# Optimization experiments

Measured on AMD Instinct MI355X. Metric: run time of the kernel, lower is better.

The kernel has to match this reference:

```python
import jax, jax.numpy as jnp
import numpy as np

B, T, C, H = 2, 2048, 1024, 16
HD = C // H  # head dim = 64


def setup_inputs() -> dict:
    key = jax.random.key(0)
    ks = jax.random.split(key, 5)
    s = 0.02  # GPT-style init scale for weights
    return {
        "x": jax.random.normal(ks[0], (B, T, C), dtype=jnp.float32),
        "Wq": jax.random.normal(ks[1], (C, C), dtype=jnp.float32) * s,
        "bq": jnp.zeros((C,), dtype=jnp.float32),
        "Wk": jax.random.normal(ks[2], (C, C), dtype=jnp.float32) * s,
        "bk": jnp.zeros((C,), dtype=jnp.float32),
        "Wv": jax.random.normal(ks[3], (C, C), dtype=jnp.float32) * s,
        "bv": jnp.zeros((C,), dtype=jnp.float32),
        "Wp": jax.random.normal(ks[4], (C, C), dtype=jnp.float32) * s,
        "bp": jnp.zeros((C,), dtype=jnp.float32),
    }


def reference(x, Wq, bq, Wk, bk, Wv, bv, Wp, bp):
    b, t, c = x.shape
    # torch nn.Linear: y = x @ W.T + b  (W is [out, in])
    def heads(W, bias):
        y = jnp.einsum("btc,oc->bto", x, W) + bias
        return y.reshape(b, t, H, HD).transpose(0, 2, 1, 3)  # [B,H,T,hd]

    q = heads(Wq, bq)
    k = heads(Wk, bk)
    v = heads(Wv, bv)

    scale = 1.0 / np.sqrt(HD).astype(np.float32)
    att = jnp.einsum("bhqd,bhkd->bhqk", q, k) * scale  # [B,H,T,T]
    causal = jnp.tril(jnp.ones((t, t), dtype=bool))
    att = jnp.where(causal[None, None], att, -jnp.inf)
    att = jax.nn.softmax(att, axis=-1)
    # attn_pdrop = 0.0 -> dropout is identity
    y = jnp.einsum("bhqk,bhkd->bhqd", att, v)  # [B,H,T,hd]
    y = y.transpose(0, 2, 1, 3).reshape(b, t, c)
    y = jnp.einsum("btc,oc->bto", y, Wp) + bp  # resid_pdrop = 0.0
    return y
```

## Files before the change

### kernel.cpp

```cpp
#include <hip/hip_runtime.h>
#include <hip/hip_bf16.h>

using bf16 = __hip_bfloat16;
typedef __attribute__((ext_vector_type(8))) short short8;
typedef __attribute__((ext_vector_type(4))) float floatx4;

#define B_  2
#define T_  2048
#define C_  1024
#define H_  16
#define HD_ 64
#define BT_ (B_*T_)
#define NX_ ((size_t)BT_*C_)
#define NW_ ((size_t)C_*C_)
#define PSTR 136
#define KSCQ 0.1803368801f

__device__ __forceinline__ void gl2lds16(const bf16* g, bf16* l) {
    __builtin_amdgcn_global_load_lds((const __attribute__((address_space(1))) unsigned int*)g,
                                     (__attribute__((address_space(3))) unsigned int*)l,
                                     16, 0, 0);
}

__global__ __launch_bounds__(256) void cvt_f32_bf16(
    const float* __restrict__ x,
    const float* __restrict__ Wq, const float* __restrict__ Wk,
    const float* __restrict__ Wv, const float* __restrict__ Wp,
    bf16* __restrict__ xb, bf16* __restrict__ wqb, bf16* __restrict__ wkb,
    bf16* __restrict__ wvb, bf16* __restrict__ wpb)
{
    size_t i4 = ((size_t)blockIdx.x * 256 + threadIdx.x) * 4;
    const float* src; bf16* dst; size_t off;
    if (i4 < NX_) { src = x; dst = xb; off = i4; }
    else {
        size_t j = i4 - NX_;
        int r = (int)(j >> 20);
        off = j & (NW_ - 1);
        src = (r==0) ? Wq : (r==1) ? Wk : (r==2) ? Wv : Wp;
        dst = (r==0) ? wqb : (r==1) ? wkb : (r==2) ? wvb : wpb;
    }
    float4 v = *(const float4*)(src + off);
    union { bf16 h[4]; uint2 u; } o;
    o.h[0] = __float2bfloat16(v.x); o.h[1] = __float2bfloat16(v.y);
    o.h[2] = __float2bfloat16(v.z); o.h[3] = __float2bfloat16(v.w);
    *(uint2*)(dst + off) = o.u;
}

__global__ __launch_bounds__(256) void qkv_gemm(
    const bf16* __restrict__ x,
    const bf16* __restrict__ Wq, const float* __restrict__ bq,
    const bf16* __restrict__ Wk, const float* __restrict__ bk,
    const bf16* __restrict__ Wv, const float* __restrict__ bv,
    bf16* __restrict__ qo, bf16* __restrict__ ko, bf16* __restrict__ vt)
{
    __shared__ __align__(16) bf16 As[128*32];
    __shared__ __align__(16) bf16 Bs[128*32];

    const int tid  = threadIdx.x;
    const int w    = tid >> 6, lane = tid & 63;
    const int g    = lane >> 4, c16 = lane & 15;
    const int wr   = w >> 1,    wc  = w & 1;
    const int mtile = blockIdx.x, ntile = blockIdx.y;
    const int wsel  = ntile >> 3;
    const bf16*  W    = (wsel==0) ? Wq : (wsel==1 ? Wk : Wv);
    const float* bias = (wsel==0) ? bq : (wsel==1 ? bk : bv);
    const float oscale = (wsel==0) ? KSCQ : 1.0f;
    const int nbase  = (ntile & 7) * 128;

    const bf16* ag = x + (size_t)(mtile*128)*C_;
    const bf16* bg = W + (size_t)nbase*C_;

    floatx4 acc[4][4] = {};

    for (int k0 = 0; k0 < C_; k0 += 32) {
        #pragma unroll
        for (int p = 0; p < 2; ++p) {
            int cb = p*256 + w*64;
            int c  = cb + lane;
            gl2lds16(ag + (size_t)(c>>2)*C_ + k0 + (c&3)*8, As + cb*8);
            gl2lds16(bg + (size_t)(c>>2)*C_ + k0 + (c&3)*8, Bs + cb*8);
        }
        __syncthreads();

        short8 af[4], bfr[4];
        #pragma unroll
        for (int i = 0; i < 4; ++i)
            af[i] = *(const short8*)(As + (wr*64 + i*16 + c16)*32 + g*8);
        #pragma unroll
        for (int j = 0; j < 4; ++j)
            bfr[j] = *(const short8*)(Bs + (wc*64 + j*16 + c16)*32 + g*8);
        #pragma unroll
        for (int i = 0; i < 4; ++i)
            #pragma unroll
            for (int j = 0; j < 4; ++j)
                acc[i][j] = __builtin_amdgcn_mfma_f32_16x16x32_bf16(af[i], bfr[j], acc[i][j], 0, 0, 0);
        __syncthreads();
    }

    #pragma unroll
    for (int i = 0; i < 4; ++i) {
        int m0 = mtile*128 + wr*64 + i*16 + g*4;
        #pragma unroll
        for (int j = 0; j < 4; ++j) {
            int n = nbase + wc*64 + j*16 + c16;
            float bvf = bias[n];
            if (wsel == 2) {
                int bb = m0 >> 11, t0 = m0 & (T_-1);
                int hh = n >> 6,  hd = n & 63;
                union { bf16 hv[4]; uint2 u; } tmp;
                #pragma unroll
                for (int r = 0; r < 4; ++r) tmp.hv[r] = __float2bfloat16(acc[i][j][r] + bvf);
                *(uint2*)(vt + ((size_t)((bb*H_ + hh)*64 + hd))*T_ + t0) = tmp.u;
            } else {
                bf16* dst = (wsel==0) ? qo : ko;
                #pragma unroll
                for (int r = 0; r < 4; ++r)
                    dst[(size_t)(m0+r)*C_ + n] = __float2bfloat16((acc[i][j][r] + bvf) * oscale);
            }
        }
    }
}

__global__ __launch_bounds__(256) void attn(
    const bf16* __restrict__ q, const bf16* __restrict__ k,
    const bf16* __restrict__ vt, bf16* __restrict__ y)
{
    __shared__ __align__(16) bf16 Ks[16*512];
    __shared__ __align__(16) bf16 Vs[16*512];
    __shared__ __align__(16) bf16 Ps[4][16*PSTR];

    const int tid = threadIdx.x, w = tid >> 6, lane = tid & 63;
    const int g = lane >> 4, c16 = lane & 15;
    const int jj = blockIdx.x, h = blockIdx.y, b = blockIdx.z;

    const bf16* kbase = k  + ((size_t)(b*T_))*C_ + h*64;
    const bf16* vbase = vt + ((size_t)(b*H_ + h))*64*T_;

    #pragma unroll 1
    for (int seg = 0; seg < 2; ++seg) {
        const int qt = seg ? jj : 31 - jj;
        const int qbase = qt*64 + w*16;
        const int nit = (qt + 2) >> 1;
        const int qglob = qbase + c16;

        short8 aq[2];
        #pragma unroll
        for (int kg = 0; kg < 2; ++kg)
            aq[kg] = *(const short8*)(q + ((size_t)(b*T_ + qglob))*C_ + h*64 + kg*32 + g*8);

        floatx4 accO[4] = {};
        float m_l = -1e30f, l_l = 0.f;

        for (int kt = 0; kt < nit; ++kt) {
            #pragma unroll
            for (int p = 0; p < 4; ++p) {
                int f = w*4 + p;
                int ctk = f >> 1, kg = f & 1;
                gl2lds16(kbase + (size_t)(kt*128 + ctk*16 + c16)*C_ + kg*32 + g*8, Ks + f*512);
                gl2lds16(vbase + (size_t)(p*16 + c16)*T_ + kt*128 + w*32 + g*8,    Vs + f*512);
            }
            __syncthreads();

            floatx4 s[8];
            #pragma unroll
            for (int ct = 0; ct < 8; ++ct) {
                floatx4 a = {0.f, 0.f, 0.f, 0.f};
                #pragma unroll
                for (int kg = 0; kg < 2; ++kg) {
                    short8 kb = *(const short8*)(Ks + (ct*2 + kg)*512 + lane*8);
                    a = __builtin_amdgcn_mfma_f32_16x16x32_bf16(kb, aq[kg], a, 0, 0, 0);
                }
                s[ct] = a;
            }

            if (kt == nit-1) {
                #pragma unroll
                for (int ct = 0; ct < 8; ++ct)
                    #pragma unroll
                    for (int r = 0; r < 4; ++r) {
                        int key = kt*128 + ct*16 + g*4 + r;
                        if (key > qglob) s[ct][r] = -1e30f;
                    }
            }

            float cm[8];
            #pragma unroll
            for (int ct = 0; ct < 8; ++ct)
                cm[ct] = fmaxf(fmaxf(s[ct][0], s[ct][1]), fmaxf(s[ct][2], s[ct][3]));
            float tmax = fmaxf(fmaxf(fmaxf(cm[0], cm[1]), fmaxf(cm[2], cm[3])),
                               fmaxf(fmaxf(cm[4], cm[5]), fmaxf(cm[6], cm[7])));
            tmax = fmaxf(tmax, __shfl_xor(tmax, 16));
            tmax = fmaxf(tmax, __shfl_xor(tmax, 32));
            float mn = fmaxf(m_l, tmax);
            float alpha = exp2f(m_l - mn);
            m_l = mn;

            float s0 = 0.f, s1 = 0.f, s2 = 0.f, s3 = 0.f;
            #pragma unroll
            for (int ct = 0; ct < 8; ++ct) {
                float p0 = exp2f(s[ct][0] - mn);
                float p1 = exp2f(s[ct][1] - mn);
                float p2 = exp2f(s[ct][2] - mn);
                float p3 = exp2f(s[ct][3] - mn);
                s0 += p0; s1 += p1; s2 += p2; s3 += p3;
                union { __hip_bfloat162 h2[2]; uint2 u; } pk;
                pk.h2[0] = __float22bfloat162_rn(float2{p0, p1});
                pk.h2[1] = __float22bfloat162_rn(float2{p2, p3});
                *(uint2*)(Ps[w] + c16*PSTR + ct*16 + g*4) = pk.u;
            }
            float tsum = (s0 + s1) + (s2 + s3);
            tsum += __shfl_xor(tsum, 16);
            tsum += __shfl_xor(tsum, 32);
            l_l = l_l*alpha + tsum;

            float ar[4];
            #pragma unroll
            for (int r = 0; r < 4; ++r) ar[r] = __shfl(alpha, g*4 + r);
            #pragma unroll
            for (int nt = 0; nt < 4; ++nt)
                #pragma unroll
                for (int r = 0; r < 4; ++r) accO[nt][r] *= ar[r];

            #pragma unroll
            for (int ks = 0; ks < 4; ++ks) {
                short8 pa = *(const short8*)(Ps[w] + c16*PSTR + ks*32 + g*8);
                #pragma unroll
                for (int nt = 0; nt < 4; ++nt) {
                    short8 vb = *(const short8*)(Vs + (ks*4 + nt)*512 + lane*8);
                    accO[nt] = __builtin_amdgcn_mfma_f32_16x16x32_bf16(pa, vb, accO[nt], 0, 0, 0);
                }
            }
            __syncthreads();
        }

        float ir[4];
        #pragma unroll
        for (int r = 0; r < 4; ++r) ir[r] = __builtin_amdgcn_rcpf(__shfl(l_l, g*4 + r));
        #pragma unroll
        for (int nt = 0; nt < 4; ++nt)
            #pragma unroll
            for (int r = 0; r < 4; ++r) {
                int row = qbase + g*4 + r;
                float o = accO[nt][r] * ir[r];
                y[((size_t)(b*T_ + row))*C_ + h*64 + nt*16 + c16] = __float2bfloat16(o);
            }
    }
}

__global__ __launch_bounds__(256) void proj_gemm(
    const bf16* __restrict__ yin, const bf16* __restrict__ Wp, const float* __restrict__ bp,
    float* __restrict__ out)
{
    __shared__ __align__(16) bf16 As[128*32];
    __shared__ __align__(16) bf16 Bs[128*32];

    const int tid = threadIdx.x;
    const int w = tid >> 6, lane = tid & 63;
    const int g = lane >> 4, c16 = lane & 15;
    const int wr = w >> 1, wc = w & 1;
    const int mtile = blockIdx.x, ntile = blockIdx.y;
    const int nbase = ntile * 128;

    const bf16* ag = yin + (size_t)(mtile*128)*C_;
    const bf16* bg = Wp  + (size_t)nbase*C_;

    floatx4 acc[4][4] = {};

    for (int k0 = 0; k0 < C_; k0 += 32) {
        #pragma unroll
        for (int p = 0; p < 2; ++p) {
            int cb = p*256 + w*64;
            int c  = cb + lane;
            gl2lds16(ag + (size_t)(c>>2)*C_ + k0 + (c&3)*8, As + cb*8);
            gl2lds16(bg + (size_t)(c>>2)*C_ + k0 + (c&3)*8, Bs + cb*8);
        }
        __syncthreads();

        short8 af[4], bfr[4];
        #pragma unroll
        for (int i = 0; i < 4; ++i)
            af[i] = *(const short8*)(As + (wr*64 + i*16 + c16)*32 + g*8);
        #pragma unroll
        for (int j = 0; j < 4; ++j)
            bfr[j] = *(const short8*)(Bs + (wc*64 + j*16 + c16)*32 + g*8);
        #pragma unroll
        for (int i = 0; i < 4; ++i)
            #pragma unroll
            for (int j = 0; j < 4; ++j)
                acc[i][j] = __builtin_amdgcn_mfma_f32_16x16x32_bf16(af[i], bfr[j], acc[i][j], 0, 0, 0);
        __syncthreads();
    }

    #pragma unroll
    for (int i = 0; i < 4; ++i) {
        int m0 = mtile*128 + wr*64 + i*16 + g*4;
        #pragma unroll
        for (int j = 0; j < 4; ++j) {
            int n = nbase + wc*64 + j*16 + c16;
            float bvf = bp[n];
            #pragma unroll
            for (int r = 0; r < 4; ++r)
                out[(size_t)(m0+r)*C_ + n] = acc[i][j][r] + bvf;
        }
    }
}

extern "C" void kernel_launch(void* const* d_in, const int* in_sizes, int n_in,
                              void* d_out, int out_size, void* d_ws, size_t ws_size,
                              hipStream_t stream) {
    const float* x  = (const float*)d_in[0];
    const float* Wq = (const float*)d_in[1];
    const float* bq = (const float*)d_in[2];
    const float* Wk = (const float*)d_in[3];
    const float* bk = (const float*)d_in[4];
    const float* Wv = (const float*)d_in[5];
    const float* bv = (const float*)d_in[6];
    const float* Wp = (const float*)d_in[7];
    const float* bp = (const float*)d_in[8];

    bf16* xb  = (bf16*)d_ws;
    bf16* wqb = xb  + NX_;
    bf16* wkb = wqb + NW_;
    bf16* wvb = wkb + NW_;
    bf16* wpb = wvb + NW_;
    bf16* qw  = wpb + NW_;
    bf16* kw  = qw  + NX_;
    bf16* vt  = kw  + NX_;
    bf16* yw  = vt  + NX_;

    const int cvt_blocks = (int)((NX_ + 4*NW_) / (4*256));
    cvt_f32_bf16<<<cvt_blocks, 256, 0, stream>>>(x, Wq, Wk, Wv, Wp, xb, wqb, wkb, wvb, wpb);
    qkv_gemm<<<dim3(32, 24), 256, 0, stream>>>(xb, wqb, bq, wkb, bk, wvb, bv, qw, kw, vt);
    attn    <<<dim3(16, H_, B_), 256, 0, stream>>>(qw, kw, vt, yw);
    proj_gemm<<<dim3(32, 8), 256, 0, stream>>>(yw, wpb, bp, (float*)d_out);
}
```

Before: 205.6 us.

## Split attention into one q-tile per block, compute row sums via MFMA

The attention kernel now launches one block per query tile (1024 blocks) instead of pairing two causal segments per block. Heads with bit 3 set reverse the tile order so heavy and light tiles interleave. The softmax denominator is accumulated with an MFMA against a ones vector instead of scalar sums and cross-lane shuffles. The P staging buffer shrinks to a 32-column chunk interleaved with the PV MFMAs, and launch bounds request 4 blocks per CU. The aim is better occupancy and less shuffle/VALU work, at the cost of losing the in-block load balancing and rounding P to bf16 before summing.

```diff
diff --git a/kernel.cpp b/kernel.cpp
--- a/kernel.cpp
+++ b/kernel.cpp
@@ -13,7 +13,7 @@
 #define BT_ (B_*T_)
 #define NX_ ((size_t)BT_*C_)
 #define NW_ ((size_t)C_*C_)
-#define PSTR 136
+#define PSTR2 40
 #define KSCQ 0.1803368801f
 
 __device__ __forceinline__ void gl2lds16(const bf16* g, bf16* l) {
@@ -121,130 +121,129 @@
     }
 }
 
-__global__ __launch_bounds__(256) void attn(
+__global__ __launch_bounds__(256, 4) void attn(
     const bf16* __restrict__ q, const bf16* __restrict__ k,
     const bf16* __restrict__ vt, bf16* __restrict__ y)
 {
     __shared__ __align__(16) bf16 Ks[16*512];
     __shared__ __align__(16) bf16 Vs[16*512];
-    __shared__ __align__(16) bf16 Ps[4][16*PSTR];
+    __shared__ __align__(16) bf16 Ps[4][16*PSTR2];
 
     const int tid = threadIdx.x, w = tid >> 6, lane = tid & 63;
     const int g = lane >> 4, c16 = lane & 15;
-    const int jj = blockIdx.x, h = blockIdx.y, b = blockIdx.z;
+    const int beta = blockIdx.x;
+    const int qraw = beta & 31, rhi = beta >> 5;
+    const int h = rhi & 15, b = rhi >> 4;
+    const int qt = (h & 8) ? 31 - qraw : qraw;
+    const int qbase = qt*64 + w*16;
+    const int nit = (qt + 2) >> 1;
+    const int qglob = qbase + c16;
 
     const bf16* kbase = k  + ((size_t)(b*T_))*C_ + h*64;
     const bf16* vbase = vt + ((size_t)(b*H_ + h))*64*T_;
 
-    #pragma unroll 1
-    for (int seg = 0; seg < 2; ++seg) {
-        const int qt = seg ? jj : 31 - jj;
-        const int qbase = qt*64 + w*16;
-        const int nit = (qt + 2) >> 1;
-        const int qglob = qbase + c16;
-
-        short8 aq[2];
-        #pragma unroll
-        for (int kg = 0; kg < 2; ++kg)
-            aq[kg] = *(const short8*)(q + ((size_t)(b*T_ + qglob))*C_ + h*64 + kg*32 + g*8);
-
-        floatx4 accO[4] = {};
-        float m_l = -1e30f, l_l = 0.f;
-
-        for (int kt = 0; kt < nit; ++kt) {
-            #pragma unroll
-            for (int p = 0; p < 4; ++p) {
-                int f = w*4 + p;
-                int ctk = f >> 1, kg = f & 1;
-                gl2lds16(kbase + (size_t)(kt*128 + ctk*16 + c16)*C_ + kg*32 + g*8, Ks + f*512);
-                gl2lds16(vbase + (size_t)(p*16 + c16)*T_ + kt*128 + w*32 + g*8,    Vs + f*512);
+    short8 aq[2];
+    #pragma unroll
+    for (int kg = 0; kg < 2; ++kg)
+        aq[kg] = *(const short8*)(q + ((size_t)(b*T_ + qglob))*C_ + h*64 + kg*32 + g*8);
+
+    const short ONEB = 0x3F80;
+    const short8 ones = {ONEB,ONEB,ONEB,ONEB,ONEB,ONEB,ONEB,ONEB};
+
+    floatx4 accO[4] = {};
+    floatx4 lacc = {};
+    float m_l = -1e30f;
+
+    for (int kt = 0; kt < nit; ++kt) {
+        #pragma unroll
+        for (int p = 0; p < 4; ++p) {
+            int f = w*4 + p;
+            int ctk = f >> 1, kg = f & 1;
+            gl2lds16(kbase + (size_t)(kt*128 + ctk*16 + c16)*C_ + kg*32 + g*8, Ks + f*512);
+            gl2lds16(vbase + (size_t)(p*16 + c16)*T_ + kt*128 + w*32 + g*8,    Vs + f*512);
+        }
+        __syncthreads();
+
+        floatx4 s[8];
+        #pragma unroll
+        for (int ct = 0; ct < 8; ++ct) {
+            floatx4 a = {0.f, 0.f, 0.f, 0.f};
+            #pragma unroll
+            for (int kg = 0; kg < 2; ++kg) {
+                short8 kb = *(const short8*)(Ks + (ct*2 + kg)*512 + lane*8);
+                a = __builtin_amdgcn_mfma_f32_16x16x32_bf16(kb, aq[kg], a, 0, 0, 0);
             }
-            __syncthreads();
-
-            floatx4 s[8];
-            #pragma unroll
-            for (int ct = 0; ct < 8; ++ct) {
-                floatx4 a = {0.f, 0.f, 0.f, 0.f};
+            s[ct] = a;
+        }
+
+        if (kt == nit-1) {
+            #pragma unroll
+            for (int ct = 0; ct < 8; ++ct)
                 #pragma unroll
-                for (int kg = 0; kg < 2; ++kg) {
-                    short8 kb = *(const short8*)(Ks + (ct*2 + kg)*512 + lane*8);
-                    a = __builtin_amdgcn_mfma_f32_16x16x32_bf16(kb, aq[kg], a, 0, 0, 0);
+                for (int r = 0; r < 4; ++r) {
+                    int key = kt*128 + ct*16 + g*4 + r;
+                    if (key > qglob) s[ct][r] = -1e30f;
                 }
-                s[ct] = a;
-            }
-
-            if (kt == nit-1) {
-                #pragma unroll
-                for (int ct = 0; ct < 8; ++ct)
-                    #pragma unroll
-                    for (int r = 0; r < 4; ++r) {
-                        int key = kt*128 + ct*16 + g*4 + r;
-                        if (key > qglob) s[ct][r] = -1e30f;
-                    }
-            }
-
-            float cm[8];
-            #pragma unroll
-            for (int ct = 0; ct < 8; ++ct)
-                cm[ct] = fmaxf(fmaxf(s[ct][0], s[ct][1]), fmaxf(s[ct][2], s[ct][3]));
-            float tmax = fmaxf(fmaxf(fmaxf(cm[0], cm[1]), fmaxf(cm[2], cm[3])),
-                               fmaxf(fmaxf(cm[4], cm[5]), fmaxf(cm[6], cm[7])));
-            tmax = fmaxf(tmax, __shfl_xor(tmax, 16));
-            tmax = fmaxf(tmax, __shfl_xor(tmax, 32));
-            float mn = fmaxf(m_l, tmax);
-            float alpha = exp2f(m_l - mn);
-            m_l = mn;
-
-            float s0 = 0.f, s1 = 0.f, s2 = 0.f, s3 = 0.f;
-            #pragma unroll
-            for (int ct = 0; ct < 8; ++ct) {
+        }
+
+        float cm[8];
+        #pragma unroll
+        for (int ct = 0; ct < 8; ++ct)
+            cm[ct] = fmaxf(fmaxf(s[ct][0], s[ct][1]), fmaxf(s[ct][2], s[ct][3]));
+        float tmax = fmaxf(fmaxf(fmaxf(cm[0], cm[1]), fmaxf(cm[2], cm[3])),
+                           fmaxf(fmaxf(cm[4], cm[5]), fmaxf(cm[6], cm[7])));
+        tmax = fmaxf(tmax, __shfl_xor(tmax, 16));
+        tmax = fmaxf(tmax, __shfl_xor(tmax, 32));
+        float mn = fmaxf(m_l, tmax);
+        float alpha = exp2f(m_l - mn);
+        m_l = mn;
+
+        float ar[4];
+        #pragma unroll
+        for (int r = 0; r < 4; ++r) ar[r] = __shfl(alpha, g*4 + r);
+        #pragma unroll
+        for (int r = 0; r < 4; ++r) {
+            lacc[r] *= ar[r];
+            #pragma unroll
+            for (int nt = 0; nt < 4; ++nt) accO[nt][r] *= ar[r];
+        }
+
+        #pragma unroll
+        for (int ks = 0; ks < 4; ++ks) {
+            #pragma unroll
+            for (int half = 0; half < 2; ++half) {
+                int ct = ks*2 + half;
                 float p0 = exp2f(s[ct][0] - mn);
                 float p1 = exp2f(s[ct][1] - mn);
                 float p2 = exp2f(s[ct][2] - mn);
                 float p3 = exp2f(s[ct][3] - mn);
-                s0 += p0; s1 += p1; s2 += p2; s3 += p3;
                 union { __hip_bfloat162 h2[2]; uint2 u; } pk;
                 pk.h2[0] = __float22bfloat162_rn(float2{p0, p1});
                 pk.h2[1] = __float22bfloat162_rn(float2{p2, p3});
-                *(uint2*)(Ps[w] + c16*PSTR + ct*16 + g*4) = pk.u;
+                *(uint2*)(Ps[w] + c16*PSTR2 + half*16 + g*4) = pk.u;
             }
-            float tsum = (s0 + s1) + (s2 + s3);
-            tsum += __shfl_xor(tsum, 16);
-            tsum += __shfl_xor(tsum, 32);
-            l_l = l_l*alpha + tsum;
-
-            float ar[4];
-            #pragma unroll
-            for (int r = 0; r < 4; ++r) ar[r] = __shfl(alpha, g*4 + r);
-            #pragma unroll
-            for (int nt = 0; nt < 4; ++nt)
-                #pragma unroll
-                for (int r = 0; r < 4; ++r) accO[nt][r] *= ar[r];
-
-            #pragma unroll
-            for (int ks = 0; ks < 4; ++ks) {
-                short8 pa = *(const short8*)(Ps[w] + c16*PSTR + ks*32 + g*8);
-                #pragma unroll
-                for (int nt = 0; nt < 4; ++nt) {
-                    short8 vb = *(const short8*)(Vs + (ks*4 + nt)*512 + lane*8);
-                    accO[nt] = __builtin_amdgcn_mfma_f32_16x16x32_bf16(pa, vb, accO[nt], 0, 0, 0);
-                }
+            short8 pa = *(const short8*)(Ps[w] + c16*PSTR2 + g*8);
+            lacc = __builtin_amdgcn_mfma_f32_16x16x32_bf16(pa, ones, lacc, 0, 0, 0);
+            #pragma unroll
+            for (int nt = 0; nt < 4; ++nt) {
+                short8 vb = *(const short8*)(Vs + (ks*4 + nt)*512 + lane*8);
+                accO[nt] = __builtin_amdgcn_mfma_f32_16x16x32_bf16(pa, vb, accO[nt], 0, 0, 0);
             }
-            __syncthreads();
-        }
-
-        float ir[4];
-        #pragma unroll
-        for (int r = 0; r < 4; ++r) ir[r] = __builtin_amdgcn_rcpf(__shfl(l_l, g*4 + r));
-        #pragma unroll
-        for (int nt = 0; nt < 4; ++nt)
-            #pragma unroll
-            for (int r = 0; r < 4; ++r) {
-                int row = qbase + g*4 + r;
-                float o = accO[nt][r] * ir[r];
-                y[((size_t)(b*T_ + row))*C_ + h*64 + nt*16 + c16] = __float2bfloat16(o);
-            }
-    }
+        }
+        __syncthreads();
+    }
+
+    float ir[4];
+    #pragma unroll
+    for (int r = 0; r < 4; ++r) ir[r] = __builtin_amdgcn_rcpf(lacc[r]);
+    #pragma unroll
+    for (int nt = 0; nt < 4; ++nt)
+        #pragma unroll
+        for (int r = 0; r < 4; ++r) {
+            int row = qbase + g*4 + r;
+            float o = accO[nt][r] * ir[r];
+            y[((size_t)(b*T_ + row))*C_ + h*64 + nt*16 + c16] = __float2bfloat16(o);
+        }
 }
 
 __global__ __launch_bounds__(256) void proj_gemm(
@@ -331,6 +330,6 @@
     const int cvt_blocks = (int)((NX_ + 4*NW_) / (4*256));
     cvt_f32_bf16<<<cvt_blocks, 256, 0, stream>>>(x, Wq, Wk, Wv, Wp, xb, wqb, wkb, wvb, wpb);
     qkv_gemm<<<dim3(32, 24), 256, 0, stream>>>(xb, wqb, bq, wkb, bk, wvb, bv, qw, kw, vt);
-    attn    <<<dim3(16, H_, B_), 256, 0, stream>>>(qw, kw, vt, yw);
+    attn    <<<1024, 256, 0, stream>>>(qw, kw, vt, yw);
     proj_gemm<<<dim3(32, 8), 256, 0, stream>>>(yw, wpb, bp, (float*)d_out);
 }
```

After: 204.1 us. No clear change (-0.7%).

## Restructure attention into single-wave blocks loading K/V directly to registers

Applied to the files above, without the earlier changes.

The attention kernel moves from 256-thread blocks that share K/V tiles through LDS and __syncthreads to 1024 single-wavefront blocks. Each block handles two 16-row query tiles (32 rows) per segment and loads K and V straight from global memory into registers. The row-sum of P is now computed with an extra MFMA against a ones vector instead of a shuffle reduction. This removes block-level barriers and LDS staging, and reuses each K/V register load across two query tiles. In exchange, global/L2 traffic per query rises because blocks no longer share K/V, register pressure is heavy (launch_bounds 64,1), and the l sum now comes from bf16-rounded P values.

```diff
diff --git a/kernel.cpp b/kernel.cpp
--- a/kernel.cpp
+++ b/kernel.cpp
@@ -121,129 +121,147 @@
     }
 }
 
-__global__ __launch_bounds__(256) void attn(
+__global__ __launch_bounds__(64, 1) void attn(
     const bf16* __restrict__ q, const bf16* __restrict__ k,
     const bf16* __restrict__ vt, bf16* __restrict__ y)
 {
-    __shared__ __align__(16) bf16 Ks[16*512];
-    __shared__ __align__(16) bf16 Vs[16*512];
-    __shared__ __align__(16) bf16 Ps[4][16*PSTR];
-
-    const int tid = threadIdx.x, w = tid >> 6, lane = tid & 63;
+    __shared__ __align__(16) bf16 Ps[2][16*PSTR];
+
+    const int lane = threadIdx.x & 63;
     const int g = lane >> 4, c16 = lane & 15;
-    const int jj = blockIdx.x, h = blockIdx.y, b = blockIdx.z;
+    const int W = blockIdx.x;
+    const int p = W & 31, bh = W >> 5;
+    const int h = bh & 15, b = bh >> 4;
 
     const bf16* kbase = k  + ((size_t)(b*T_))*C_ + h*64;
     const bf16* vbase = vt + ((size_t)(b*H_ + h))*64*T_;
+    const short ONEB = 0x3F80;
+    const short8 ones = {ONEB,ONEB,ONEB,ONEB,ONEB,ONEB,ONEB,ONEB};
 
     #pragma unroll 1
     for (int seg = 0; seg < 2; ++seg) {
-        const int qt = seg ? jj : 31 - jj;
-        const int qbase = qt*64 + w*16;
-        const int nit = (qt + 2) >> 1;
-        const int qglob = qbase + c16;
-
-        short8 aq[2];
-        #pragma unroll
-        for (int kg = 0; kg < 2; ++kg)
-            aq[kg] = *(const short8*)(q + ((size_t)(b*T_ + qglob))*C_ + h*64 + kg*32 + g*8);
-
-        floatx4 accO[4] = {};
-        float m_l = -1e30f, l_l = 0.f;
-
+        const int j  = seg ? p : 63 - p;
+        const int q0 = j * 32;
+        const int nit = (j >> 2) + 1;
+
+        short8 aq[2][2];
+        #pragma unroll
+        for (int rt = 0; rt < 2; ++rt)
+            #pragma unroll
+            for (int kg = 0; kg < 2; ++kg)
+                aq[rt][kg] = *(const short8*)(q + ((size_t)(b*T_ + q0 + rt*16 + c16))*C_
+                                                + h*64 + kg*32 + g*8);
+
+        floatx4 accO[2][4] = {};
+        floatx4 lacc[2] = {};
+        float m_l[2] = {-1e30f, -1e30f};
+
+        #pragma unroll 1
         for (int kt = 0; kt < nit; ++kt) {
-            #pragma unroll
-            for (int p = 0; p < 4; ++p) {
-                int f = w*4 + p;
-                int ctk = f >> 1, kg = f & 1;
-                gl2lds16(kbase + (size_t)(kt*128 + ctk*16 + c16)*C_ + kg*32 + g*8, Ks + f*512);
-                gl2lds16(vbase + (size_t)(p*16 + c16)*T_ + kt*128 + w*32 + g*8,    Vs + f*512);
+            const bf16* kp = kbase + (size_t)(kt*128 + c16)*C_ + g*8;
+            short8 kb[8][2];
+            #pragma unroll
+            for (int ct = 0; ct < 8; ++ct)
+                #pragma unroll
+                for (int kg = 0; kg < 2; ++kg)
+                    kb[ct][kg] = *(const short8*)(kp + (size_t)(ct*16)*C_ + kg*32);
+            const bf16* vp = vbase + (size_t)c16*T_ + kt*128 + g*8;
+            short8 vb[4][4];
+            #pragma unroll
+            for (int ks = 0; ks < 4; ++ks)
+                #pragma unroll
+                for (int nt = 0; nt < 4; ++nt)
+                    vb[ks][nt] = *(const short8*)(vp + (size_t)(nt*16)*T_ + ks*32);
+
+            floatx4 s[2][8];
+            #pragma unroll
+            for (int rt = 0; rt < 2; ++rt)
+                #pragma unroll
+                for (int ct = 0; ct < 8; ++ct) {
+                    floatx4 a = {0.f, 0.f, 0.f, 0.f};
+                    a = __builtin_amdgcn_mfma_f32_16x16x32_bf16(kb[ct][0], aq[rt][0], a, 0, 0, 0);
+                    a = __builtin_amdgcn_mfma_f32_16x16x32_bf16(kb[ct][1], aq[rt][1], a, 0, 0, 0);
+                    s[rt][ct] = a;
+                }
+
+            if (kt == nit-1) {
+                #pragma unroll
+                for (int rt = 0; rt < 2; ++rt) {
+                    int qglob = q0 + rt*16 + c16;
+                    #pragma unroll
+                    for (int ct = 0; ct < 8; ++ct)
+                        #pragma unroll
+                        for (int r = 0; r < 4; ++r) {
+                            int key = kt*128 + ct*16 + g*4 + r;
+                            if (key > qglob) s[rt][ct][r] = -1e30f;
+                        }
+                }
             }
-            __syncthreads();
-
-            floatx4 s[8];
-            #pragma unroll
-            for (int ct = 0; ct < 8; ++ct) {
-                floatx4 a = {0.f, 0.f, 0.f, 0.f};
-                #pragma unroll
-                for (int kg = 0; kg < 2; ++kg) {
-                    short8 kb = *(const short8*)(Ks + (ct*2 + kg)*512 + lane*8);
-                    a = __builtin_amdgcn_mfma_f32_16x16x32_bf16(kb, aq[kg], a, 0, 0, 0);
-                }
-                s[ct] = a;
+
+            #pragma unroll
+            for (int rt = 0; rt < 2; ++rt) {
+                float cm[8];
+                #pragma unroll
+                for (int ct = 0; ct < 8; ++ct)
+                    cm[ct] = fmaxf(fmaxf(s[rt][ct][0], s[rt][ct][1]),
+                                   fmaxf(s[rt][ct][2], s[rt][ct][3]));
+                float tmax = fmaxf(fmaxf(fmaxf(cm[0], cm[1]), fmaxf(cm[2], cm[3])),
+                                   fmaxf(fmaxf(cm[4], cm[5]), fmaxf(cm[6], cm[7])));
+                tmax = fmaxf(tmax, __shfl_xor(tmax, 16));
+                tmax = fmaxf(tmax, __shfl_xor(tmax, 32));
+                float mn = fmaxf(m_l[rt], tmax);
+                float alpha = exp2f(m_l[rt] - mn);
+                m_l[rt] = mn;
+
+                float ar[4];
+                #pragma unroll
+                for (int r = 0; r < 4; ++r) ar[r] = __shfl(alpha, g*4 + r);
+                #pragma unroll
+                for (int r = 0; r < 4; ++r) {
+                    lacc[rt][r] *= ar[r];
+                    #pragma unroll
+                    for (int nt = 0; nt < 4; ++nt) accO[rt][nt][r] *= ar[r];
+                }
+
+                #pragma unroll
+                for (int ct = 0; ct < 8; ++ct) {
+                    float p0 = exp2f(s[rt][ct][0] - mn);
+                    float p1 = exp2f(s[rt][ct][1] - mn);
+                    float p2 = exp2f(s[rt][ct][2] - mn);
+                    float p3 = exp2f(s[rt][ct][3] - mn);
+                    union { __hip_bfloat162 h2[2]; uint2 u; } pk;
+                    pk.h2[0] = __float22bfloat162_rn(float2{p0, p1});
+                    pk.h2[1] = __float22bfloat162_rn(float2{p2, p3});
+                    *(uint2*)(Ps[rt] + c16*PSTR + ct*16 + g*4) = pk.u;
+                }
+                short8 pa[4];
+                #pragma unroll
+                for (int ks = 0; ks < 4; ++ks)
+                    pa[ks] = *(const short8*)(Ps[rt] + c16*PSTR + ks*32 + g*8);
+                #pragma unroll
+                for (int ks = 0; ks < 4; ++ks) {
+                    lacc[rt] = __builtin_amdgcn_mfma_f32_16x16x32_bf16(pa[ks], ones, lacc[rt], 0, 0, 0);
+                    #pragma unroll
+                    for (int nt = 0; nt < 4; ++nt)
+                        accO[rt][nt] = __builtin_amdgcn_mfma_f32_16x16x32_bf16(pa[ks], vb[ks][nt], accO[rt][nt], 0, 0, 0);
+                }
             }
-
-            if (kt == nit-1) {
-                #pragma unroll
-                for (int ct = 0; ct < 8; ++ct)
-                    #pragma unroll
-                    for (int r = 0; r < 4; ++r) {
-                        int key = kt*128 + ct*16 + g*4 + r;
-                        if (key > qglob) s[ct][r] = -1e30f;
-                    }
-            }
-
-            float cm[8];
-            #pragma unroll
-            for (int ct = 0; ct < 8; ++ct)
-                cm[ct] = fmaxf(fmaxf(s[ct][0], s[ct][1]), fmaxf(s[ct][2], s[ct][3]));
-            float tmax = fmaxf(fmaxf(fmaxf(cm[0], cm[1]), fmaxf(cm[2], cm[3])),
-                               fmaxf(fmaxf(cm[4], cm[5]), fmaxf(cm[6], cm[7])));
-            tmax = fmaxf(tmax, __shfl_xor(tmax, 16));
-            tmax = fmaxf(tmax, __shfl_xor(tmax, 32));
-            float mn = fmaxf(m_l, tmax);
-            float alpha = exp2f(m_l - mn);
-            m_l = mn;
-
-            float s0 = 0.f, s1 = 0.f, s2 = 0.f, s3 = 0.f;
-            #pragma unroll
-            for (int ct = 0; ct < 8; ++ct) {
-                float p0 = exp2f(s[ct][0] - mn);
-                float p1 = exp2f(s[ct][1] - mn);
-                float p2 = exp2f(s[ct][2] - mn);
-                float p3 = exp2f(s[ct][3] - mn);
-                s0 += p0; s1 += p1; s2 += p2; s3 += p3;
-                union { __hip_bfloat162 h2[2]; uint2 u; } pk;
-                pk.h2[0] = __float22bfloat162_rn(float2{p0, p1});
-                pk.h2[1] = __float22bfloat162_rn(float2{p2, p3});
-                *(uint2*)(Ps[w] + c16*PSTR + ct*16 + g*4) = pk.u;
-            }
-            float tsum = (s0 + s1) + (s2 + s3);
-            tsum += __shfl_xor(tsum, 16);
-            tsum += __shfl_xor(tsum, 32);
-            l_l = l_l*alpha + tsum;
-
-            float ar[4];
-            #pragma unroll
-            for (int r = 0; r < 4; ++r) ar[r] = __shfl(alpha, g*4 + r);
+        }
+
+        #pragma unroll
+        for (int rt = 0; rt < 2; ++rt) {
+            float ir[4];
+            #pragma unroll
+            for (int r = 0; r < 4; ++r) ir[r] = __builtin_amdgcn_rcpf(lacc[rt][r]);
             #pragma unroll
             for (int nt = 0; nt < 4; ++nt)
                 #pragma unroll
-                for (int r = 0; r < 4; ++r) accO[nt][r] *= ar[r];
-
-            #pragma unroll
-            for (int ks = 0; ks < 4; ++ks) {
-                short8 pa = *(const short8*)(Ps[w] + c16*PSTR + ks*32 + g*8);
-                #pragma unroll
-                for (int nt = 0; nt < 4; ++nt) {
-                    short8 vb = *(const short8*)(Vs + (ks*4 + nt)*512 + lane*8);
-                    accO[nt] = __builtin_amdgcn_mfma_f32_16x16x32_bf16(pa, vb, accO[nt], 0, 0, 0);
-                }
-            }
-            __syncthreads();
-        }
-
-        float ir[4];
-        #pragma unroll
-        for (int r = 0; r < 4; ++r) ir[r] = __builtin_amdgcn_rcpf(__shfl(l_l, g*4 + r));
-        #pragma unroll
-        for (int nt = 0; nt < 4; ++nt)
-            #pragma unroll
-            for (int r = 0; r < 4; ++r) {
-                int row = qbase + g*4 + r;
-                float o = accO[nt][r] * ir[r];
-                y[((size_t)(b*T_ + row))*C_ + h*64 + nt*16 + c16] = __float2bfloat16(o);
-            }
+                for (int r = 0; r < 4; ++r) {
+                    int row = q0 + rt*16 + g*4 + r;
+                    float o = accO[rt][nt][r] * ir[r];
+                    y[((size_t)(b*T_ + row))*C_ + h*64 + nt*16 + c16] = __float2bfloat16(o);
+                }
+        }
     }
 }
 
@@ -331,6 +349,6 @@
     const int cvt_blocks = (int)((NX_ + 4*NW_) / (4*256));
     cvt_f32_bf16<<<cvt_blocks, 256, 0, stream>>>(x, Wq, Wk, Wv, Wp, xb, wqb, wkb, wvb, wpb);
     qkv_gemm<<<dim3(32, 24), 256, 0, stream>>>(xb, wqb, bq, wkb, bk, wvb, bv, qw, kw, vt);
-    attn    <<<dim3(16, H_, B_), 256, 0, stream>>>(qw, kw, vt, yw);
+    attn    <<<1024, 64, 0, stream>>>(qw, kw, vt, yw);
     proj_gemm<<<dim3(32, 8), 256, 0, stream>>>(yw, wpb, bp, (float*)d_out);
 }
```

Result: slower. 229.0 us (+11.4%).
